# Kernel optimization log

Hardware: AMD Instinct MI355X
Metric: run time of the kernel (lower is better)

Reference implementation:

```python
import jax, jax.numpy as jnp
import numpy as np

WS = 16      # window_size
HEADS = 8    # num_heads


def setup_inputs() -> dict:
    key = jax.random.key(0)
    ks = jax.random.split(key, 3)
    B, C, H, W = 16, 512, 64, 64
    x = jax.random.normal(ks[0], (B, C, H, W), dtype=jnp.float32)
    in_proj_w = jax.random.normal(ks[1], (3 * C, C), dtype=jnp.float32) * 0.02
    in_proj_b = jnp.zeros((3 * C,), dtype=jnp.float32)
    out_w = jax.random.normal(ks[2], (C, C), dtype=jnp.float32) * 0.02
    out_b = jnp.zeros((C,), dtype=jnp.float32)
    return {"x": x, "in_proj_w": in_proj_w, "in_proj_b": in_proj_b,
            "out_w": out_w, "out_b": out_b}


def reference(x, in_proj_w, in_proj_b, out_w, out_b):
    B, C, H, W = x.shape
    pad_h = (-H) % WS
    pad_w = (-W) % WS
    x = jnp.pad(x, ((0, 0), (0, 0), (0, pad_h), (0, pad_w)))
    Hp, Wp = x.shape[2], x.shape[3]
    nH, nW = Hp // WS, Wp // WS
    # window partition: (B,C,Hp,Wp) -> (B*nH*nW, WS*WS, C)
    xw = x.reshape(B, C, nH, WS, nW, WS)
    xw = xw.transpose(0, 2, 4, 3, 5, 1).reshape(B * nH * nW, WS * WS, C)
    # torch MHA default batch_first=False: dim0 = seq (L = B*nH*nW), dim1 = batch (N = WS*WS)
    L, N, _ = xw.shape
    d = C // HEADS
    qkv = xw @ in_proj_w.T + in_proj_b            # (L, N, 3C)
    q, k, v = jnp.split(qkv, 3, axis=-1)
    q = q.reshape(L, N, HEADS, d) * (d ** -0.5)
    k = k.reshape(L, N, HEADS, d)
    v = v.reshape(L, N, HEADS, d)
    scores = jnp.einsum('lnhd,mnhd->nhlm', q, k)  # (N, H, L, L)
    attn = jax.nn.softmax(scores, axis=-1)
    o = jnp.einsum('nhlm,mnhd->lnhd', attn, v).reshape(L, N, C)
    o = o @ out_w.T + out_b                       # (L, N, C)
    # window reverse: -> (B, C, Hp, Wp)
    o = o.reshape(B, nH, nW, WS, WS, C).transpose(0, 5, 1, 3, 2, 4)
    o = o.reshape(B, C, Hp, Wp)
    return o[:, :, :H, :W]
```

## Files before the change

### kernel.cpp

```cpp
#include <hip/hip_runtime.h>
#include <stdint.h>
#include <stddef.h>
#include <math.h>


typedef __bf16 bf16;
typedef __attribute__((ext_vector_type(8))) __bf16 bf16x8;
typedef __attribute__((ext_vector_type(4))) __bf16 bf16x4;
typedef __attribute__((ext_vector_type(4))) float f32x4;

#define MFMA16(A, B, C) __builtin_amdgcn_mfma_f32_16x16x32_bf16((A), (B), (C), 0, 0, 0)

__device__ __forceinline__ float fast_exp2(float x) { return __builtin_amdgcn_exp2f(x); }

__device__ __forceinline__ int aswz(int n, int c) {
  int g = (c >> 3) ^ ((n >> 4) & 7) ^ (n & 7);
  return n * 512 + (g << 3) + (c & 7);
}

__global__ void cvt_pack(const float* __restrict__ w1f, const float* __restrict__ w2f,
                         bf16* __restrict__ w1p, bf16* __restrict__ w2p) {
  int i = blockIdx.x * 256 + threadIdx.x;
  const float* src;
  bf16* dst;
  if (i < 98304) { src = w1f; dst = w1p; }
  else           { src = w2f; dst = w2p; i -= 98304; }
  int lane = i & 63;
  int ks   = (i >> 6) & 15;
  int t    = i >> 10;
  int cout = t * 16 + (lane & 15);
  int c0   = ks * 32 + (lane >> 4) * 8;
  float4 a = *(const float4*)(src + (size_t)cout * 512 + c0);
  float4 b = *(const float4*)(src + (size_t)cout * 512 + c0 + 4);
  bf16x8 r;
  r[0] = (bf16)a.x; r[1] = (bf16)a.y; r[2] = (bf16)a.z; r[3] = (bf16)a.w;
  r[4] = (bf16)b.x; r[5] = (bf16)b.y; r[6] = (bf16)b.z; r[7] = (bf16)b.w;
  *(bf16x8*)(dst + (size_t)i * 8) = r;
}

__global__ void __launch_bounds__(256, 2) gemm_qkv(
    const float* __restrict__ x, const bf16* __restrict__ w1p,
    const float* __restrict__ b1,
    bf16* __restrict__ qo, bf16* __restrict__ ko, bf16* __restrict__ vo) {
  extern __shared__ bf16 Al[];
  bf16* Ep = Al + 64 * 512;
  const int tid = threadIdx.x;
  const int bm  = blockIdx.x;
  const int l   = bm >> 2;
  const int n0  = (bm & 3) << 6;
  const int b   = l >> 4, ih = (l >> 2) & 3, iw = l & 3;
  const int h0  = ih * 16 + (n0 >> 4);
  const int w0  = iw * 16;

  for (int j = 0; j < 32; ++j) {
    int f4  = j * 256 + tid;
    int c   = f4 >> 4;
    int qq  = f4 & 15;
    int wsh = qq >> 2;
    int w4  = (qq & 3) << 2;
    float4 xf = *(const float4*)(x + (((b * 512 + c) * 64 + h0 + wsh) * 64 + w0 + w4));
    int nb = wsh * 16 + w4;
    Al[aswz(nb + 0, c)] = (bf16)xf.x;
    Al[aswz(nb + 1, c)] = (bf16)xf.y;
    Al[aswz(nb + 2, c)] = (bf16)xf.z;
    Al[aswz(nb + 3, c)] = (bf16)xf.w;
  }
  __syncthreads();

  const int wave = tid >> 6, lane = tid & 63;
  const int l15 = lane & 15, quad = lane >> 4;
  bf16* Epw = Ep + wave * 16 * 72;
  const f32x4 fz = {0.f, 0.f, 0.f, 0.f};

  for (int nc = 0; nc < 6; ++nc) {
    const int t0w = nc * 256 + wave * 64;
    const int tb  = t0w >> 4;
    f32x4 acc[4][4];
#pragma unroll
    for (int a = 0; a < 4; ++a)
#pragma unroll
      for (int c2 = 0; c2 < 4; ++c2) acc[a][c2] = fz;

    bf16x8 bfr[4];
#pragma unroll
    for (int ct = 0; ct < 4; ++ct)
      bfr[ct] = *(const bf16x8*)&w1p[((size_t)((tb + ct) * 16 + 0) * 64 + lane) * 8];
#pragma unroll
    for (int ks = 0; ks < 16; ++ks) {
      bf16x8 bnx[4];
      if (ks < 15) {
#pragma unroll
        for (int ct = 0; ct < 4; ++ct)
          bnx[ct] = *(const bf16x8*)&w1p[((size_t)((tb + ct) * 16 + ks + 1) * 64 + lane) * 8];
      }
      bf16x8 af[4];
#pragma unroll
      for (int lt = 0; lt < 4; ++lt)
        af[lt] = *(const bf16x8*)&Al[aswz(lt * 16 + l15, ks * 32 + quad * 8)];
#pragma unroll
      for (int lt = 0; lt < 4; ++lt)
#pragma unroll
        for (int ct = 0; ct < 4; ++ct)
          acc[lt][ct] = MFMA16(af[lt], bfr[ct], acc[lt][ct]);
#pragma unroll
      for (int ct = 0; ct < 4; ++ct) bfr[ct] = bnx[ct];
    }

    const int which = t0w >> 9;
    const int hh = (t0w & 511) >> 6;
    bf16* dst = (which == 0) ? qo : (which == 1) ? ko : vo;
    const float scale = (which == 0) ? 0.125f : 1.0f;
    float bias[4];
#pragma unroll
    for (int ct = 0; ct < 4; ++ct) bias[ct] = b1[t0w + ct * 16 + l15];

#pragma unroll
    for (int lt = 0; lt < 4; ++lt) {
#pragma unroll
      for (int ct = 0; ct < 4; ++ct)
#pragma unroll
        for (int r = 0; r < 4; ++r)
          Epw[(quad * 4 + r) * 72 + ct * 16 + l15] =
              (bf16)((acc[lt][ct][r] + bias[ct]) * scale);
      const int rr = lane >> 3, ch8 = (lane & 7) * 8;
#pragma unroll
      for (int half = 0; half < 2; ++half) {
        int row = half * 8 + rr;
        bf16x8 vv = *(const bf16x8*)&Epw[row * 72 + ch8];
        int n = n0 + lt * 16 + row;
        *(bf16x8*)&dst[((size_t)(n * 8 + hh) * 256 + l) * 64 + ch8] = vv;
      }
    }
  }
}

__global__ void __launch_bounds__(512, 2) attn_win(
    bf16* __restrict__ qio, const bf16* __restrict__ kg, const bf16* __restrict__ vg) {
  extern __shared__ bf16 sm[];
  bf16* Kl = sm;
  bf16* Vt = sm + 256 * 72;
  bf16* Pl = Vt + 64 * 264;
  const int tid = threadIdx.x;
  const int bb = blockIdx.x;
  const int n = bb >> 3, h = bb & 7;
  const size_t base = (size_t)(n * 8 + h) * 16384;
  const bf16* Kg = kg + base;
  const bf16* Vg = vg + base;
  bf16* Qg = qio + base;

  for (int j = 0; j < 4; ++j) {
    int cc = j * 512 + tid;
    int m = cc >> 3, dc = cc & 7;
    bf16x8 t = *(const bf16x8*)(Kg + m * 64 + dc * 8);
    *(bf16x8*)&Kl[m * 72 + dc * 8] = t;
  }
  for (int j = 0; j < 4; ++j) {
    int cc = j * 512 + tid;
    int dc = cc >> 8, m = cc & 255;
    bf16x8 t = *(const bf16x8*)(Vg + m * 64 + dc * 8);
#pragma unroll
    for (int s = 0; s < 8; ++s) Vt[(dc * 8 + s) * 264 + m] = t[s];
  }

  const int wave = tid >> 6, lane = tid & 63;
  const int l15 = lane & 15, quad = lane >> 4;
  const int lb = wave * 32;
  bf16* Pw = Pl + wave * 16 * 264;

  bf16x8 qf[2][2];
#pragma unroll
  for (int lt = 0; lt < 2; ++lt)
#pragma unroll
    for (int ks = 0; ks < 2; ++ks)
      qf[lt][ks] = *(const bf16x8*)(Qg + (lb + lt * 16 + l15) * 64 + ks * 32 + quad * 8);

  __syncthreads();

  const f32x4 fz = {0.f, 0.f, 0.f, 0.f};
  const float LOG2E = 1.44269504088896340736f;
  for (int lt = 0; lt < 2; ++lt) {
    f32x4 s[16];
#pragma unroll
    for (int mt = 0; mt < 16; ++mt) s[mt] = fz;
#pragma unroll
    for (int mt = 0; mt < 16; ++mt)
#pragma unroll
      for (int ks = 0; ks < 2; ++ks) {
        bf16x8 kf = *(const bf16x8*)&Kl[(mt * 16 + l15) * 72 + ks * 32 + quad * 8];
        s[mt] = MFMA16(qf[lt][ks], kf, s[mt]);
      }
    float rmax[4], rsum[4];
#pragma unroll
    for (int r = 0; r < 4; ++r) {
      float mx = s[0][r];
#pragma unroll
      for (int mt = 1; mt < 16; ++mt) mx = fmaxf(mx, s[mt][r]);
#pragma unroll
      for (int xo = 1; xo < 16; xo <<= 1) mx = fmaxf(mx, __shfl_xor(mx, xo, 16));
      rmax[r] = mx;
      rsum[r] = 0.f;
    }
#pragma unroll
    for (int mt = 0; mt < 16; ++mt) {
#pragma unroll
      for (int r = 0; r < 4; ++r) {
        float p = fast_exp2((s[mt][r] - rmax[r]) * LOG2E);
        bf16 pb = (bf16)p;
        rsum[r] += (float)pb;
        Pw[(quad * 4 + r) * 264 + mt * 16 + l15] = pb;
      }
    }
#pragma unroll
    for (int r = 0; r < 4; ++r)
#pragma unroll
      for (int xo = 1; xo < 16; xo <<= 1) rsum[r] += __shfl_xor(rsum[r], xo, 16);

    bf16x8 pf[8];
#pragma unroll
    for (int mk = 0; mk < 8; ++mk)
      pf[mk] = *(const bf16x8*)&Pw[l15 * 264 + mk * 32 + quad * 8];
    f32x4 of[4];
#pragma unroll
    for (int dt = 0; dt < 4; ++dt) of[dt] = fz;
#pragma unroll
    for (int dt = 0; dt < 4; ++dt)
#pragma unroll
      for (int mk = 0; mk < 8; ++mk) {
        bf16x8 vf = *(const bf16x8*)&Vt[(dt * 16 + l15) * 264 + mk * 32 + quad * 8];
        of[dt] = MFMA16(pf[mk], vf, of[dt]);
      }
    float inv[4];
#pragma unroll
    for (int r = 0; r < 4; ++r) inv[r] = 1.0f / rsum[r];

    bf16* Ew = Pw;
#pragma unroll
    for (int dt = 0; dt < 4; ++dt)
#pragma unroll
      for (int r = 0; r < 4; ++r)
        Ew[(quad * 4 + r) * 72 + dt * 16 + l15] = (bf16)(of[dt][r] * inv[r]);
    const int rr = lane >> 3, ch8 = (lane & 7) * 8;
#pragma unroll
    for (int half = 0; half < 2; ++half) {
      int row = half * 8 + rr;
      bf16x8 vv = *(const bf16x8*)&Ew[row * 72 + ch8];
      *(bf16x8*)(Qg + (lb + lt * 16 + row) * 64 + ch8) = vv;
    }
  }
}

__global__ void __launch_bounds__(256, 2) gemm_out(
    const bf16* __restrict__ og, const bf16* __restrict__ w2p,
    const float* __restrict__ b2, float* __restrict__ out) {
  extern __shared__ bf16 Al[];
  const int tid = threadIdx.x;
  const int bm = blockIdx.x;
  const int l = bm >> 2;
  const int n0 = (bm & 3) << 6;
  const int b = l >> 4, ih = (l >> 2) & 3, iw = l & 3;

  for (int j = 0; j < 16; ++j) {
    int cc = j * 256 + tid;
    int nl = cc >> 6;
    int ch = cc & 63;
    int hh = ch >> 3, d8 = (ch & 7) * 8;
    bf16x8 t = *(const bf16x8*)(og + ((size_t)((n0 + nl) * 8 + hh) * 256 + l) * 64 + d8);
    *(bf16x8*)&Al[aswz(nl, ch * 8)] = t;
  }
  __syncthreads();

  const int wave = tid >> 6, lane = tid & 63;
  const int l15 = lane & 15, quad = lane >> 4;
  const f32x4 fz = {0.f, 0.f, 0.f, 0.f};

  for (int nc = 0; nc < 2; ++nc) {
    const int t0w = nc * 256 + wave * 64;
    const int tb  = t0w >> 4;
    f32x4 acc[4][4];
#pragma unroll
    for (int a = 0; a < 4; ++a)
#pragma unroll
      for (int c2 = 0; c2 < 4; ++c2) acc[a][c2] = fz;

    bf16x8 bfr[4];
#pragma unroll
    for (int ct = 0; ct < 4; ++ct)
      bfr[ct] = *(const bf16x8*)&w2p[((size_t)((tb + ct) * 16 + 0) * 64 + lane) * 8];
#pragma unroll
    for (int ks = 0; ks < 16; ++ks) {
      bf16x8 bnx[4];
      if (ks < 15) {
#pragma unroll
        for (int ct = 0; ct < 4; ++ct)
          bnx[ct] = *(const bf16x8*)&w2p[((size_t)((tb + ct) * 16 + ks + 1) * 64 + lane) * 8];
      }
      bf16x8 af[4];
#pragma unroll
      for (int lt = 0; lt < 4; ++lt)
        af[lt] = *(const bf16x8*)&Al[aswz(lt * 16 + l15, ks * 32 + quad * 8)];
#pragma unroll
      for (int lt = 0; lt < 4; ++lt)
#pragma unroll
        for (int ct = 0; ct < 4; ++ct)
          acc[lt][ct] = MFMA16(bfr[ct], af[lt], acc[lt][ct]);
#pragma unroll
      for (int ct = 0; ct < 4; ++ct) bfr[ct] = bnx[ct];
    }

#pragma unroll
    for (int ct = 0; ct < 4; ++ct) {
      float4 bias4 = *(const float4*)&b2[t0w + ct * 16 + quad * 4];
#pragma unroll
      for (int lt = 0; lt < 4; ++lt) {
        const int nbase = n0 + lt * 16;
        const int wsh = nbase >> 4;
        size_t rowbase = (((size_t)b * 512) * 64 + (size_t)ih * 16 + wsh) * 64 + iw * 16 + l15;
#pragma unroll
        for (int r = 0; r < 4; ++r) {
          int cout = t0w + ct * 16 + quad * 4 + r;
          out[rowbase + (size_t)cout * 4096] = acc[lt][ct][r] + ((const float*)&bias4)[r];
        }
      }
    }
  }
}

extern "C" void kernel_launch(void* const* d_in, const int* in_sizes, int n_in,
                              void* d_out, int out_size, void* d_ws, size_t ws_size,
                              hipStream_t stream) {
  (void)in_sizes; (void)n_in; (void)out_size; (void)ws_size;
  const float* x   = (const float*)d_in[0];
  const float* w1f = (const float*)d_in[1];
  const float* b1  = (const float*)d_in[2];
  const float* w2f = (const float*)d_in[3];
  const float* b2  = (const float*)d_in[4];
  float* out = (float*)d_out;

  char* ws = (char*)d_ws;
  bf16* q   = (bf16*)(ws);
  bf16* k   = (bf16*)(ws + 67108864ull);
  bf16* v   = (bf16*)(ws + 134217728ull);
  bf16* w1p = (bf16*)(ws + 201326592ull);
  bf16* w2p = (bf16*)(ws + 201326592ull + 1572864ull);

  const int LDS_QKV  = (64 * 512 + 4 * 16 * 72) * 2;
  const int LDS_ATTN = (256 * 72 + 64 * 264 + 8 * 16 * 264) * 2;
  const int LDS_OUT  = 64 * 512 * 2;
  hipFuncSetAttribute(reinterpret_cast<const void*>(gemm_qkv),
                      hipFuncAttributeMaxDynamicSharedMemorySize, LDS_QKV);
  hipFuncSetAttribute(reinterpret_cast<const void*>(attn_win),
                      hipFuncAttributeMaxDynamicSharedMemorySize, LDS_ATTN);
  hipFuncSetAttribute(reinterpret_cast<const void*>(gemm_out),
                      hipFuncAttributeMaxDynamicSharedMemorySize, LDS_OUT);

  hipLaunchKernelGGL(cvt_pack, dim3(512), dim3(256), 0, stream, w1f, w2f, w1p, w2p);
  hipLaunchKernelGGL(gemm_qkv, dim3(1024), dim3(256), LDS_QKV, stream, x, w1p, b1, q, k, v);
  hipLaunchKernelGGL(attn_win, dim3(2048), dim3(512), LDS_ATTN, stream, q, k, v);
  hipLaunchKernelGGL(gemm_out, dim3(1024), dim3(256), LDS_OUT, stream, q, w2p, b2, out);
}
```

Measured before the change: 615.3 us.

## Cut attention LDS footprint: read K from global, chunk P through small buffer

The attention kernel stops staging K in shared memory and reads K fragments straight from global memory. The softmax probabilities are now written and consumed in 64-column chunks interleaved with the PV MFMAs, so each wave's P buffer shrinks from 16x264 to 16x72. Q fragments are loaded per row-tile. Together these cut LDS per block from about 139KB to about 52KB, and the launch bound is raised to 4 blocks per CU to allow more occupancy. The cost is repeated K reads from global or L2 by all 8 waves, plus tighter register limits.

```diff
diff --git a/kernel.cpp b/kernel.cpp
--- a/kernel.cpp
+++ b/kernel.cpp
@@ -134,12 +134,11 @@
   }
 }
 
-__global__ void __launch_bounds__(512, 2) attn_win(
+__global__ void __launch_bounds__(512, 4) attn_win(
     bf16* __restrict__ qio, const bf16* __restrict__ kg, const bf16* __restrict__ vg) {
   extern __shared__ bf16 sm[];
-  bf16* Kl = sm;
-  bf16* Vt = sm + 256 * 72;
-  bf16* Pl = Vt + 64 * 264;
+  bf16* Vt = sm;
+  bf16* Pl = sm + 64 * 264;
   const int tid = threadIdx.x;
   const int bb = blockIdx.x;
   const int n = bb >> 3, h = bb & 7;
@@ -150,35 +149,27 @@
 
   for (int j = 0; j < 4; ++j) {
     int cc = j * 512 + tid;
-    int m = cc >> 3, dc = cc & 7;
-    bf16x8 t = *(const bf16x8*)(Kg + m * 64 + dc * 8);
-    *(bf16x8*)&Kl[m * 72 + dc * 8] = t;
-  }
-  for (int j = 0; j < 4; ++j) {
-    int cc = j * 512 + tid;
     int dc = cc >> 8, m = cc & 255;
     bf16x8 t = *(const bf16x8*)(Vg + m * 64 + dc * 8);
 #pragma unroll
     for (int s = 0; s < 8; ++s) Vt[(dc * 8 + s) * 264 + m] = t[s];
   }
+  __syncthreads();
 
   const int wave = tid >> 6, lane = tid & 63;
   const int l15 = lane & 15, quad = lane >> 4;
   const int lb = wave * 32;
-  bf16* Pw = Pl + wave * 16 * 264;
-
-  bf16x8 qf[2][2];
-#pragma unroll
-  for (int lt = 0; lt < 2; ++lt)
-#pragma unroll
-    for (int ks = 0; ks < 2; ++ks)
-      qf[lt][ks] = *(const bf16x8*)(Qg + (lb + lt * 16 + l15) * 64 + ks * 32 + quad * 8);
-
-  __syncthreads();
+  bf16* Pw = Pl + wave * 16 * 72;
 
   const f32x4 fz = {0.f, 0.f, 0.f, 0.f};
   const float LOG2E = 1.44269504088896340736f;
   for (int lt = 0; lt < 2; ++lt) {
+    const int row0 = lb + lt * 16;
+    bf16x8 qf[2];
+#pragma unroll
+    for (int ks = 0; ks < 2; ++ks)
+      qf[ks] = *(const bf16x8*)(Qg + (row0 + l15) * 64 + ks * 32 + quad * 8);
+
     f32x4 s[16];
 #pragma unroll
     for (int mt = 0; mt < 16; ++mt) s[mt] = fz;
@@ -186,9 +177,10 @@
     for (int mt = 0; mt < 16; ++mt)
 #pragma unroll
       for (int ks = 0; ks < 2; ++ks) {
-        bf16x8 kf = *(const bf16x8*)&Kl[(mt * 16 + l15) * 72 + ks * 32 + quad * 8];
-        s[mt] = MFMA16(qf[lt][ks], kf, s[mt]);
-      }
+        bf16x8 kf = *(const bf16x8*)(Kg + (mt * 16 + l15) * 64 + ks * 32 + quad * 8);
+        s[mt] = MFMA16(qf[ks], kf, s[mt]);
+      }
+
     float rmax[4], rsum[4];
 #pragma unroll
     for (int r = 0; r < 4; ++r) {
@@ -200,51 +192,55 @@
       rmax[r] = mx;
       rsum[r] = 0.f;
     }
-#pragma unroll
-    for (int mt = 0; mt < 16; ++mt) {
-#pragma unroll
-      for (int r = 0; r < 4; ++r) {
-        float p = fast_exp2((s[mt][r] - rmax[r]) * LOG2E);
-        bf16 pb = (bf16)p;
-        rsum[r] += (float)pb;
-        Pw[(quad * 4 + r) * 264 + mt * 16 + l15] = pb;
-      }
-    }
+
+    f32x4 of[4];
+#pragma unroll
+    for (int dt = 0; dt < 4; ++dt) of[dt] = fz;
+
+#pragma unroll
+    for (int mc = 0; mc < 4; ++mc) {
+#pragma unroll
+      for (int mi = 0; mi < 4; ++mi) {
+        const int mt = mc * 4 + mi;
+#pragma unroll
+        for (int r = 0; r < 4; ++r) {
+          float p = fast_exp2((s[mt][r] - rmax[r]) * LOG2E);
+          bf16 pb = (bf16)p;
+          rsum[r] += (float)pb;
+          Pw[(quad * 4 + r) * 72 + mi * 16 + l15] = pb;
+        }
+      }
+#pragma unroll
+      for (int mkl = 0; mkl < 2; ++mkl) {
+        bf16x8 pf = *(const bf16x8*)&Pw[l15 * 72 + mkl * 32 + quad * 8];
+        const int mk = mc * 2 + mkl;
+#pragma unroll
+        for (int dt = 0; dt < 4; ++dt) {
+          bf16x8 vf = *(const bf16x8*)&Vt[(dt * 16 + l15) * 264 + mk * 32 + quad * 8];
+          of[dt] = MFMA16(pf, vf, of[dt]);
+        }
+      }
+    }
+
 #pragma unroll
     for (int r = 0; r < 4; ++r)
 #pragma unroll
       for (int xo = 1; xo < 16; xo <<= 1) rsum[r] += __shfl_xor(rsum[r], xo, 16);
-
-    bf16x8 pf[8];
-#pragma unroll
-    for (int mk = 0; mk < 8; ++mk)
-      pf[mk] = *(const bf16x8*)&Pw[l15 * 264 + mk * 32 + quad * 8];
-    f32x4 of[4];
-#pragma unroll
-    for (int dt = 0; dt < 4; ++dt) of[dt] = fz;
+    float inv[4];
+#pragma unroll
+    for (int r = 0; r < 4; ++r) inv[r] = 1.0f / rsum[r];
+
 #pragma unroll
     for (int dt = 0; dt < 4; ++dt)
 #pragma unroll
-      for (int mk = 0; mk < 8; ++mk) {
-        bf16x8 vf = *(const bf16x8*)&Vt[(dt * 16 + l15) * 264 + mk * 32 + quad * 8];
-        of[dt] = MFMA16(pf[mk], vf, of[dt]);
-      }
-    float inv[4];
-#pragma unroll
-    for (int r = 0; r < 4; ++r) inv[r] = 1.0f / rsum[r];
-
-    bf16* Ew = Pw;
-#pragma unroll
-    for (int dt = 0; dt < 4; ++dt)
-#pragma unroll
       for (int r = 0; r < 4; ++r)
-        Ew[(quad * 4 + r) * 72 + dt * 16 + l15] = (bf16)(of[dt][r] * inv[r]);
+        Pw[(quad * 4 + r) * 72 + dt * 16 + l15] = (bf16)(of[dt][r] * inv[r]);
     const int rr = lane >> 3, ch8 = (lane & 7) * 8;
 #pragma unroll
     for (int half = 0; half < 2; ++half) {
       int row = half * 8 + rr;
-      bf16x8 vv = *(const bf16x8*)&Ew[row * 72 + ch8];
-      *(bf16x8*)(Qg + (lb + lt * 16 + row) * 64 + ch8) = vv;
+      bf16x8 vv = *(const bf16x8*)&Pw[row * 72 + ch8];
+      *(bf16x8*)(Qg + (row0 + row) * 64 + ch8) = vv;
     }
   }
 }
@@ -344,7 +340,7 @@
   bf16* w2p = (bf16*)(ws + 201326592ull + 1572864ull);
 
   const int LDS_QKV  = (64 * 512 + 4 * 16 * 72) * 2;
-  const int LDS_ATTN = (256 * 72 + 64 * 264 + 8 * 16 * 264) * 2;
+  const int LDS_ATTN = (64 * 264 + 8 * 16 * 72) * 2;
   const int LDS_OUT  = 64 * 512 * 2;
   hipFuncSetAttribute(reinterpret_cast<const void*>(gemm_qkv),
                       hipFuncAttributeMaxDynamicSharedMemorySize, LDS_QKV);
```

Result: slower. 857.3 us (+39.3%).
